# Kernel optimization log

Measured on AMD Instinct MI355X. Metric: run time of the kernel, lower is better.

The kernel has to match this reference:

```python
import jax, jax.numpy as jnp
from jax import lax
import numpy as np

EPS = 1e-6

def setup_inputs() -> dict:
    key = jax.random.key(0)
    ks = jax.random.split(key, 6)
    b, c, h, w = 16, 512, 64, 64
    x = jax.random.normal(ks[0], (b, c, h, w), dtype=jnp.float32)
    s = jax.random.normal(ks[1], (b, c, 1, h * w), dtype=jnp.float32)
    z = jax.random.uniform(ks[2], (b, 1, c, 1), dtype=jnp.float32)
    wq = jax.random.normal(ks[3], (1, 1, 5), dtype=jnp.float32) * 0.2
    wk = jax.random.normal(ks[4], (1, 1, 5), dtype=jnp.float32) * 0.2
    wv = jax.random.normal(ks[5], (512, 1, 3, 3), dtype=jnp.float32) * 0.2
    return {"x": x, "s": s, "z": z, "wq": wq, "wk": wk, "wv": wv}

def _elu_fm(t):
    # elu feature map: elu(t) + 1 (strictly positive)
    return jax.nn.elu(t) + 1.0

def reference(x, s, z, wq, wk, wv):
    b, c, h, w = x.shape
    # adaptive avg pool to 1x1 -> [b,1,c] channel descriptor
    y = jnp.mean(x, axis=(2, 3)).reshape(b, 1, c)
    # ECA-style conv1d over channel axis (kernel 5, SAME padding)
    Q = lax.conv_general_dilated(y, wq, (1,), [(2, 2)],
                                 dimension_numbers=("NCW", "OIW", "NCW"))
    K = lax.conv_general_dilated(y, wk, (1,), [(2, 2)],
                                 dimension_numbers=("NCW", "OIW", "NCW"))
    # depthwise 3x3 conv on V
    V = lax.conv_general_dilated(x, wv, (1, 1), [(1, 1), (1, 1)],
                                 dimension_numbers=("NCHW", "OIHW", "NCHW"),
                                 feature_group_count=c)
    Qf = _elu_fm(Q)[:, 0, :]          # [b, c]
    Kf = _elu_fm(K)[:, 0, :]          # [b, c]
    Vf = V.reshape(b, c, h * w)       # [b, c, hw]
    # KV outer product per channel (c-dim of K is size-1 in einsum, so scalar * row)
    s_new = s + (Kf[:, :, None] * Vf)[:, :, None, :]   # [b, c, 1, hw]
    z_new = z + Kf.reshape(b, 1, c, 1)                 # [b, 1, c, 1]
    qz = 1.0 / (Qf * (z_new[:, 0, :, 0] + EPS))        # [b, c]
    out = (Qf * qz)[:, :, None] * s_new[:, :, 0, :]    # [b, c, hw]
    return out.reshape(b, c, h, w), s_new, z_new
```

## Files before the change

### kernel.cpp

```cpp
#include <hip/hip_runtime.h>
#include <math.h>

#define EPS 1e-6f

__global__ __launch_bounds__(256) void mean_kernel(const float* __restrict__ x,
                                                   float* __restrict__ y) {
    int plane = blockIdx.x;
    const float4* xp = (const float4*)(x + (size_t)plane * 4096);
    int t = threadIdx.x;
    float sum = 0.f;
#pragma unroll
    for (int k = 0; k < 4; ++k) {
        float4 v = xp[t + k * 256];
        sum += v.x + v.y + v.z + v.w;
    }
#pragma unroll
    for (int off = 32; off > 0; off >>= 1)
        sum += __shfl_down(sum, off, 64);
    __shared__ float lds[4];
    if ((t & 63) == 0) lds[t >> 6] = sum;
    __syncthreads();
    if (t == 0) {
        float s = lds[0] + lds[1] + lds[2] + lds[3];
        y[plane] = s * (1.0f / 4096.0f);
    }
}

__global__ __launch_bounds__(256) void qk_kernel(const float* __restrict__ y,
                                                 const float* __restrict__ z,
                                                 const float* __restrict__ wq,
                                                 const float* __restrict__ wk,
                                                 float* __restrict__ kf_out,
                                                 float* __restrict__ factor_out,
                                                 float* __restrict__ znew_out) {
    int gid = blockIdx.x * blockDim.x + threadIdx.x;
    int b = gid >> 9;
    int ch = gid & 511;
    float q = 0.f, k = 0.f;
#pragma unroll
    for (int i = 0; i < 5; ++i) {
        int cc = ch + i - 2;
        float yv = (cc >= 0 && cc < 512) ? y[b * 512 + cc] : 0.f;
        q += yv * wq[i];
        k += yv * wk[i];
    }
    float qf = (q > 0.f) ? (q + 1.f) : expf(q);
    float kf = (k > 0.f) ? (k + 1.f) : expf(k);
    float zn = z[gid] + kf;
    znew_out[gid] = zn;
    float qz = 1.0f / (qf * (zn + EPS));
    kf_out[gid] = kf;
    factor_out[gid] = qf * qz;
}

__global__ __launch_bounds__(256) void fused_kernel(
    const float* __restrict__ x, const float* __restrict__ s,
    const float* __restrict__ wv, const float* __restrict__ kf_arr,
    const float* __restrict__ factor_arr, float* __restrict__ out,
    float* __restrict__ s_new) {
    int plane = blockIdx.x >> 2;
    int chunk = blockIdx.x & 3;
    int ch = plane & 511;
    float kf = kf_arr[plane];
    float fac = factor_arr[plane];
    const float* wvp = wv + ch * 9;
    float w00 = wvp[0], w01 = wvp[1], w02 = wvp[2];
    float w10 = wvp[3], w11 = wvp[4], w12 = wvp[5];
    float w20 = wvp[6], w21 = wvp[7], w22 = wvp[8];

    int ty = threadIdx.x >> 4;
    int tx = threadIdx.x & 15;
    int row = chunk * 16 + ty;
    int col0 = tx << 2;

    const float* xp = x + (size_t)plane * 4096;

    float r0[6], r1[6], r2[6];
    {
        const int rows[3] = {row - 1, row, row + 1};
        float* bufs[3] = {r0, r1, r2};
#pragma unroll
        for (int rr = 0; rr < 3; ++rr) {
            int r = rows[rr];
            float* buf = bufs[rr];
            if (r < 0 || r >= 64) {
#pragma unroll
                for (int m = 0; m < 6; ++m) buf[m] = 0.f;
            } else {
                const float* rp = xp + r * 64 + col0;
                buf[0] = (col0 == 0) ? 0.f : rp[-1];
                float4 v = *(const float4*)rp;
                buf[1] = v.x;
                buf[2] = v.y;
                buf[3] = v.z;
                buf[4] = v.w;
                buf[5] = (col0 + 4 >= 64) ? 0.f : rp[4];
            }
        }
    }

    float vj[4];
#pragma unroll
    for (int j = 0; j < 4; ++j) {
        vj[j] = r0[j] * w00 + r0[j + 1] * w01 + r0[j + 2] * w02 +
                r1[j] * w10 + r1[j + 1] * w11 + r1[j + 2] * w12 +
                r2[j] * w20 + r2[j + 1] * w21 + r2[j + 2] * w22;
    }

    size_t off = (size_t)plane * 4096 + (size_t)row * 64 + col0;
    float4 s4 = *(const float4*)(s + off);
    float4 sn;
    sn.x = s4.x + kf * vj[0];
    sn.y = s4.y + kf * vj[1];
    sn.z = s4.z + kf * vj[2];
    sn.w = s4.w + kf * vj[3];
    *(float4*)(s_new + off) = sn;
    float4 o;
    o.x = fac * sn.x;
    o.y = fac * sn.y;
    o.z = fac * sn.z;
    o.w = fac * sn.w;
    *(float4*)(out + off) = o;
}

extern "C" void kernel_launch(void* const* d_in, const int* in_sizes, int n_in,
                              void* d_out, int out_size, void* d_ws,
                              size_t ws_size, hipStream_t stream) {
    const float* x  = (const float*)d_in[0];
    const float* s  = (const float*)d_in[1];
    const float* z  = (const float*)d_in[2];
    const float* wq = (const float*)d_in[3];
    const float* wk = (const float*)d_in[4];
    const float* wv = (const float*)d_in[5];

    float* out   = (float*)d_out;
    float* s_new = out + 33554432;
    float* z_new = s_new + 33554432;

    float* ws     = (float*)d_ws;
    float* y      = ws;
    float* kf     = ws + 8192;
    float* factor = ws + 16384;

    mean_kernel<<<8192, 256, 0, stream>>>(x, y);
    qk_kernel<<<32, 256, 0, stream>>>(y, z, wq, wk, kf, factor, z_new);
    fused_kernel<<<32768, 256, 0, stream>>>(x, s, wv, kf, factor, out, s_new);
}
```

Measured before the change: 470.9 us.

## Stage whole input plane in LDS for depthwise conv, one block per plane

The fused kernel now assigns one block per 64x64 plane and first copies the entire plane into a 16KB shared-memory tile. Each thread computes four rows of the 3x3 depthwise stencil from LDS, using mask multipliers for the borders. This removes the redundant halo and neighbour global loads (unaligned scalar reads and overlapping rows between blocks) of the old scheme. The cost is 16KB of LDS per block, which may limit occupancy, plus a sync barrier and a serial load phase before compute.

Measured after the change: 454.8 us. -3.4%, faster.

```diff
diff --git a/kernel.cpp b/kernel.cpp
--- a/kernel.cpp
+++ b/kernel.cpp
@@ -58,8 +58,9 @@
     const float* __restrict__ wv, const float* __restrict__ kf_arr,
     const float* __restrict__ factor_arr, float* __restrict__ out,
     float* __restrict__ s_new) {
-    int plane = blockIdx.x >> 2;
-    int chunk = blockIdx.x & 3;
+    __shared__ float tile[4096];
+
+    int plane = blockIdx.x;
     int ch = plane & 511;
     float kf = kf_arr[plane];
     float fac = factor_arr[plane];
@@ -68,59 +69,75 @@
     float w10 = wvp[3], w11 = wvp[4], w12 = wvp[5];
     float w20 = wvp[6], w21 = wvp[7], w22 = wvp[8];
 
-    int ty = threadIdx.x >> 4;
-    int tx = threadIdx.x & 15;
-    int row = chunk * 16 + ty;
+    int t = threadIdx.x;
+    const float4* xp4 = (const float4*)(x + (size_t)plane * 4096);
+    float4* t4 = (float4*)tile;
+#pragma unroll
+    for (int k = 0; k < 4; ++k)
+        t4[t + k * 256] = xp4[t + k * 256];
+    __syncthreads();
+
+    int ty = t >> 4;
+    int tx = t & 15;
     int col0 = tx << 2;
 
-    const float* xp = x + (size_t)plane * 4096;
+    float lm = (col0 == 0) ? 0.f : 1.f;
+    float rm = (col0 == 60) ? 0.f : 1.f;
+    int li = (col0 == 0) ? 0 : col0 - 1;
+    int ri = (col0 == 60) ? 63 : col0 + 4;
 
-    float r0[6], r1[6], r2[6];
-    {
-        const int rows[3] = {row - 1, row, row + 1};
-        float* bufs[3] = {r0, r1, r2};
 #pragma unroll
-        for (int rr = 0; rr < 3; ++rr) {
-            int r = rows[rr];
-            float* buf = bufs[rr];
-            if (r < 0 || r >= 64) {
-#pragma unroll
-                for (int m = 0; m < 6; ++m) buf[m] = 0.f;
-            } else {
-                const float* rp = xp + r * 64 + col0;
-                buf[0] = (col0 == 0) ? 0.f : rp[-1];
-                float4 v = *(const float4*)rp;
-                buf[1] = v.x;
-                buf[2] = v.y;
-                buf[3] = v.z;
-                buf[4] = v.w;
-                buf[5] = (col0 + 4 >= 64) ? 0.f : rp[4];
-            }
-        }
+    for (int rr = 0; rr < 4; ++rr) {
+        int row = ty + rr * 16;
+        int rcB = row * 64;
+        int rmB = (row == 0) ? rcB : rcB - 64;
+        int rpB = (row == 63) ? rcB : rcB + 64;
+        float tm = (row == 0) ? 0.f : 1.f;
+        float bm = (row == 63) ? 0.f : 1.f;
+
+        float4 tq = *(const float4*)(tile + rmB + col0);
+        float t0 = tile[rmB + li] * (tm * lm);
+        float t1 = tq.x * tm, t2 = tq.y * tm, t3 = tq.z * tm, t4v = tq.w * tm;
+        float t5 = tile[rmB + ri] * (tm * rm);
+
+        float4 cq = *(const float4*)(tile + rcB + col0);
+        float c0 = tile[rcB + li] * lm;
+        float c1 = cq.x, c2 = cq.y, c3 = cq.z, c4 = cq.w;
+        float c5 = tile[rcB + ri] * rm;
+
+        float4 bq = *(const float4*)(tile + rpB + col0);
+        float b0 = tile[rpB + li] * (bm * lm);
+        float b1 = bq.x * bm, b2 = bq.y * bm, b3 = bq.z * bm, b4 = bq.w * bm;
+        float b5 = tile[rpB + ri] * (bm * rm);
+
+        float v0 = t0 * w00 + t1 * w01 + t2 * w02 +
+                   c0 * w10 + c1 * w11 + c2 * w12 +
+                   b0 * w20 + b1 * w21 + b2 * w22;
+        float v1 = t1 * w00 + t2 * w01 + t3 * w02 +
+                   c1 * w10 + c2 * w11 + c3 * w12 +
+                   b1 * w20 + b2 * w21 + b3 * w22;
+        float v2 = t2 * w00 + t3 * w01 + t4v * w02 +
+                   c2 * w10 + c3 * w11 + c4 * w12 +
+                   b2 * w20 + b3 * w21 + b4 * w22;
+        float v3 = t3 * w00 + t4v * w01 + t5 * w02 +
+                   c3 * w10 + c4 * w11 + c5 * w12 +
+                   b3 * w20 + b4 * w21 + b5 * w22;
+
+        size_t off = (size_t)plane * 4096 + (size_t)rcB + col0;
+        float4 s4 = *(const float4*)(s + off);
+        float4 sn;
+        sn.x = s4.x + kf * v0;
+        sn.y = s4.y + kf * v1;
+        sn.z = s4.z + kf * v2;
+        sn.w = s4.w + kf * v3;
+        *(float4*)(s_new + off) = sn;
+        float4 o;
+        o.x = fac * sn.x;
+        o.y = fac * sn.y;
+        o.z = fac * sn.z;
+        o.w = fac * sn.w;
+        *(float4*)(out + off) = o;
     }
-
-    float vj[4];
-#pragma unroll
-    for (int j = 0; j < 4; ++j) {
-        vj[j] = r0[j] * w00 + r0[j + 1] * w01 + r0[j + 2] * w02 +
-                r1[j] * w10 + r1[j + 1] * w11 + r1[j + 2] * w12 +
-                r2[j] * w20 + r2[j + 1] * w21 + r2[j + 2] * w22;
-    }
-
-    size_t off = (size_t)plane * 4096 + (size_t)row * 64 + col0;
-    float4 s4 = *(const float4*)(s + off);
-    float4 sn;
-    sn.x = s4.x + kf * vj[0];
-    sn.y = s4.y + kf * vj[1];
-    sn.z = s4.z + kf * vj[2];
-    sn.w = s4.w + kf * vj[3];
-    *(float4*)(s_new + off) = sn;
-    float4 o;
-    o.x = fac * sn.x;
-    o.y = fac * sn.y;
-    o.z = fac * sn.z;
-    o.w = fac * sn.w;
-    *(float4*)(out + off) = o;
 }
 
 extern "C" void kernel_launch(void* const* d_in, const int* in_sizes, int n_in,
@@ -144,5 +161,5 @@
 
     mean_kernel<<<8192, 256, 0, stream>>>(x, y);
     qk_kernel<<<32, 256, 0, stream>>>(y, z, wq, wk, kf, factor, z_new);
-    fused_kernel<<<32768, 256, 0, stream>>>(x, s, wv, kf, factor, out, s_new);
+    fused_kernel<<<8192, 256, 0, stream>>>(x, s, wv, kf, factor, out, s_new);
 }
```
